# Performance work log

Hardware: AMD Instinct MI355X
Metric: run time of the kernel (lower is better)

## Reference

```python
import jax, jax.numpy as jnp
import numpy as np
import math

EMB, QK, V, HEAD = 512, 64, 64, 8
B, S = 8, 2048

def setup_inputs() -> dict:
    key = jax.random.key(0)
    ks = jax.random.split(key, 10)
    sc = 1.0 / math.sqrt(EMB)
    return {
        "x_q": jax.random.normal(ks[0], (B, S, EMB), jnp.float32),
        "x_k_v": jax.random.normal(ks[1], (B, S, EMB), jnp.float32),
        "attn_mask": jax.random.randint(ks[2], (B, S, S), 0, 2, jnp.int32),
        "w_q": jax.random.normal(ks[3], (HEAD * QK, EMB), jnp.float32) * sc,
        "b_q": jax.random.normal(ks[4], (HEAD * QK,), jnp.float32) * sc,
        "w_k": jax.random.normal(ks[5], (HEAD * QK, EMB), jnp.float32) * sc,
        "b_k": jax.random.normal(ks[6], (HEAD * QK,), jnp.float32) * sc,
        "w_v": jax.random.normal(ks[7], (HEAD * V, EMB), jnp.float32) * sc,
        "b_v": jax.random.normal(ks[8], (HEAD * V,), jnp.float32) * sc,
    }

def reference(x_q, x_k_v, attn_mask, w_q, b_q, w_k, b_k, w_v, b_v):
    Bq, Sq, _ = x_q.shape
    Skv = x_k_v.shape[1]
    # linear projections (torch Linear: x @ W.T + b)
    q = (x_q @ w_q.T + b_q).reshape(Bq, Sq, HEAD, QK)     # [B,Sq,H,Dk]
    k = (x_k_v @ w_k.T + b_k).reshape(Bq, Skv, HEAD, QK)  # [B,Skv,H,Dk]
    v = (x_k_v @ w_v.T + b_v).reshape(Bq, Skv, HEAD, V)   # [B,Skv,H,Dv]
    # scores [B,H,Sq,Skv]
    attn = jnp.einsum("bqhd,bkhd->bhqk", q, k) / math.sqrt(QK)
    mask = attn_mask[:, None, :, :].astype(bool)
    attn = jnp.where(mask, jnp.float32(-1e9), attn)
    attn = jax.nn.softmax(attn, axis=-1)
    z = jnp.einsum("bhqk,bkhd->bqhd", attn, v)            # [B,Sq,H,Dv]
    return z.reshape(Bq, Sq, HEAD * V)
```

## Files before the change

### kernel.cpp

```cpp
#include <hip/hip_runtime.h>
#include <hip/hip_bf16.h>
#include <math.h>

typedef float  f32x4  __attribute__((ext_vector_type(4)));
typedef float  f32x16 __attribute__((ext_vector_type(16)));
typedef short  s16x8  __attribute__((ext_vector_type(8)));
typedef __bf16 bf16x8 __attribute__((ext_vector_type(8)));
typedef unsigned int u32;
typedef unsigned int u32x4 __attribute__((ext_vector_type(4)));
typedef unsigned short u16;
typedef unsigned long long u64;

#define DEVI static __device__ __forceinline__

#if defined(__has_builtin) && __has_builtin(__builtin_amdgcn_exp2f)
#define EXP2(x) __builtin_amdgcn_exp2f(x)
#else
#define EXP2(x) exp2f(x)
#endif

DEVI u32 cvtpk(float lo, float hi) {
  u32 r;
  asm("v_cvt_pk_bf16_f32 %0, %1, %2" : "=v"(r) : "v"(lo), "v"(hi));
  return r;
}

DEVI f32x4 mfma_bf16(s16x8 a, s16x8 b, f32x4 c) {
  return __builtin_amdgcn_mfma_f32_16x16x32_bf16(
      __builtin_bit_cast(bf16x8, a), __builtin_bit_cast(bf16x8, b), c, 0, 0, 0);
}

DEVI f32x16 mfma32(s16x8 a, s16x8 b, f32x16 c) {
  return __builtin_amdgcn_mfma_f32_32x32x16_bf16(
      __builtin_bit_cast(bf16x8, a), __builtin_bit_cast(bf16x8, b), c, 0, 0, 0);
}

DEVI void gload_lds16(const void* g, void* l) {
  __builtin_amdgcn_global_load_lds(
      (const __attribute__((address_space(1))) void*)g,
      (__attribute__((address_space(3))) void*)l, 16, 0, 0);
}

__global__ __launch_bounds__(256)
void mask_pack(const int* __restrict__ mask, u64* __restrict__ mp) {
  const int t = threadIdx.x, lane = t & 63;
  const int gw = blockIdx.x * 4 + (t >> 6);
  const int kt = gw & 31, q = (gw >> 5) & 2047, b = gw >> 16;
  int mv = mask[((size_t)b * 2048 + q) * 2048 + kt * 64 + lane];
  u64 bits = __ballot(mv == 0);
  if (lane == 0) mp[((size_t)b * 32 + kt) * 2048 + q] = bits;
}

__global__ __launch_bounds__(256, 2)
void qkv_proj(const float* __restrict__ xq, const float* __restrict__ xkv,
              const float* __restrict__ wq, const float* __restrict__ bq,
              const float* __restrict__ wk, const float* __restrict__ bk,
              const float* __restrict__ wv, const float* __restrict__ bv,
              u16* __restrict__ Qo, u16* __restrict__ Ko, u16* __restrict__ VTo)
{
  __shared__ __align__(16) char smem[128 * 272];
  char* lds_a = smem;
  char* lds_b = smem + 8192;

  const int t = threadIdx.x, lane = t & 63, w = t >> 6;
  const int z = blockIdx.z;
  const float* X  = (z == 0) ? xq : xkv;
  const float* W  = (z == 0) ? wq : (z == 1 ? wk : wv);
  const float* Bv = (z == 0) ? bq : (z == 1 ? bk : bv);

  const int m0 = blockIdx.x * 128, n0 = blockIdx.y * 128;
  const int wr = w >> 1, wc = w & 1, g = lane >> 4, q15 = lane & 15;
  const int srow = t >> 1, shalf = t & 1;

  f32x4 acc[4][4];
  #pragma unroll
  for (int i = 0; i < 4; ++i)
    #pragma unroll
    for (int j = 0; j < 4; ++j) acc[i][j] = (f32x4){0.f, 0.f, 0.f, 0.f};

  const float* gA = X + (size_t)(m0 + srow) * 512 + shalf * 16;
  const float* gB = W + (size_t)(n0 + srow) * 512 + shalf * 16;
  const int wbyte = srow * 64;
  const int sw = (srow & 3) << 4;

  #pragma unroll 1
  for (int kt = 0; kt < 16; ++kt) {
    float4 fa[4], fb[4];
    #pragma unroll
    for (int j = 0; j < 4; ++j) {
      fa[j] = *(const float4*)(gA + kt * 32 + j * 4);
      fb[j] = *(const float4*)(gB + kt * 32 + j * 4);
    }
    __syncthreads();
    const float* pfa = (const float*)fa;
    const float* pfb = (const float*)fb;
    #pragma unroll
    for (int half = 0; half < 2; ++half) {
      u32x4 wa, wb;
      #pragma unroll
      for (int e2 = 0; e2 < 4; ++e2) {
        wa[e2] = cvtpk(pfa[half * 8 + 2 * e2], pfa[half * 8 + 2 * e2 + 1]);
        wb[e2] = cvtpk(pfb[half * 8 + 2 * e2], pfb[half * 8 + 2 * e2 + 1]);
      }
      *(u32x4*)(lds_a + wbyte + ((shalf * 32 + half * 16) ^ sw)) = wa;
      *(u32x4*)(lds_b + wbyte + ((shalf * 32 + half * 16) ^ sw)) = wb;
    }
    __syncthreads();
    s16x8 afr[4], bfr[4];
    #pragma unroll
    for (int mi = 0; mi < 4; ++mi) {
      int row = wr * 64 + mi * 16 + q15;
      afr[mi] = *(const s16x8*)(lds_a + row * 64 + ((g * 16) ^ ((row & 3) << 4)));
    }
    #pragma unroll
    for (int ni = 0; ni < 4; ++ni) {
      int row = wc * 64 + ni * 16 + q15;
      bfr[ni] = *(const s16x8*)(lds_b + row * 64 + ((g * 16) ^ ((row & 3) << 4)));
    }
    #pragma unroll
    for (int mi = 0; mi < 4; ++mi)
      #pragma unroll
      for (int ni = 0; ni < 4; ++ni)
        acc[mi][ni] = mfma_bf16(afr[mi], bfr[ni], acc[mi][ni]);
  }

  float bias[4];
  #pragma unroll
  for (int ni = 0; ni < 4; ++ni) bias[ni] = Bv[n0 + wc * 64 + ni * 16 + q15];

  if (z < 2) {
    u16* Out = z ? Ko : Qo;
    const float scale = z ? 1.0f : 0.18033688011112042f;
    #pragma unroll
    for (int mi = 0; mi < 4; ++mi)
      #pragma unroll
      for (int ni = 0; ni < 4; ++ni)
        #pragma unroll
        for (int r = 0; r < 4; r += 2) {
          int m = m0 + wr * 64 + mi * 16 + g * 4 + r;
          int n = n0 + wc * 64 + ni * 16 + q15;
          u32 pk = cvtpk((acc[mi][ni][r] + bias[ni]) * scale,
                         (acc[mi][ni][r + 1] + bias[ni]) * scale);
          Out[(size_t)m * 512 + n]       = (u16)pk;
          Out[(size_t)(m + 1) * 512 + n] = (u16)(pk >> 16);
        }
  } else {
    __syncthreads();
    #pragma unroll
    for (int mi = 0; mi < 4; ++mi)
      #pragma unroll
      for (int ni = 0; ni < 4; ++ni)
        #pragma unroll
        for (int r = 0; r < 4; r += 2) {
          int ml = wr * 64 + mi * 16 + g * 4 + r;
          int nl = wc * 64 + ni * 16 + q15;
          *(u32*)(smem + nl * 272 + ml * 2) =
              cvtpk(acc[mi][ni][r] + bias[ni], acc[mi][ni][r + 1] + bias[ni]);
        }
    __syncthreads();
    const int b  = m0 >> 11;
    const int s0 = m0 & 2047;
    #pragma unroll
    for (int nn = 0; nn < 2; ++nn) {
      int n  = nn * 64 + (t >> 2);
      int q4 = t & 3;
      u16* dst = VTo + (size_t)(b * 512 + n0 + n) * 2048 + s0 + q4 * 32;
      #pragma unroll
      for (int jj = 0; jj < 4; ++jj)
        *(s16x8*)(dst + jj * 8) = *(const s16x8*)(smem + n * 272 + q4 * 64 + jj * 16);
    }
  }
}

__global__ __launch_bounds__(128, 2)
void attn_fwd(const u16* __restrict__ Q, const u16* __restrict__ K,
              const u16* __restrict__ VT, const u64* __restrict__ MP,
              float* __restrict__ out)
{
  __shared__ __align__(16) char lds_k[2][8192];
  __shared__ __align__(16) char lds_v[2][8192];

  const int bid = blockIdx.x;
  const int h = bid & 7, b = (bid >> 3) & 7, qt = bid >> 6;
  const int t = threadIdx.x, lane = t & 63, w = t >> 6;
  const int l31 = lane & 31, hi = lane >> 5;
  const int qbase = qt * 128 + w * 64;
  const int swz = (l31 & 7) << 4;

  s16x8 qfa[4], qfb[4];
  #pragma unroll
  for (int j = 0; j < 4; ++j) {
    qfa[j] = *(const s16x8*)(Q + (size_t)(b * 2048 + qbase + l31) * 512
                               + h * 64 + j * 16 + hi * 8);
    qfb[j] = *(const s16x8*)(Q + (size_t)(b * 2048 + qbase + 32 + l31) * 512
                               + h * 64 + j * 16 + hi * 8);
  }
  asm volatile("" ::: "memory");

  f32x16 oA0 = {0.f,0.f,0.f,0.f,0.f,0.f,0.f,0.f,0.f,0.f,0.f,0.f,0.f,0.f,0.f,0.f};
  f32x16 oA1 = oA0, oB0 = oA0, oB1 = oA0, zA = oA0, zB = oA0;
  const f32x16 ZZ = oA0;
  const s16x8 onesf = {0x3F80,0x3F80,0x3F80,0x3F80,0x3F80,0x3F80,0x3F80,0x3F80};

  const int srow8 = lane >> 3, slot = lane & 7;
  const int sx = (slot ^ srow8) * 8;
  const u16* kPtr[4];
  const u16* vPtr[4];
  #pragma unroll
  for (int i = 0; i < 4; ++i) {
    int rl = w * 32 + i * 8 + srow8;
    kPtr[i] = K  + (size_t)(b * 2048 + rl) * 512 + h * 64 + sx;
    vPtr[i] = VT + (size_t)(b * 512 + h * 64 + rl) * 2048 + sx;
  }
  const u64* mpP = MP + (size_t)b * 32 * 2048 + qbase + l31;

  #pragma unroll
  for (int i = 0; i < 4; ++i) gload_lds16(kPtr[i], &lds_k[0][(w * 4 + i) * 1024]);
  #pragma unroll
  for (int i = 0; i < 4; ++i) gload_lds16(vPtr[i], &lds_v[0][(w * 4 + i) * 1024]);
  asm volatile("" ::: "memory");
  u64 pm0 = mpP[0], pm1 = mpP[32];

  #pragma unroll 1
  for (int kt = 0; kt < 32; ++kt) {
    const int cur = kt & 1;
    const u64 kwA = pm0, kwB = pm1;
    asm volatile("s_waitcnt vmcnt(0) lgkmcnt(0)" ::: "memory");
    __builtin_amdgcn_sched_barrier(0);
    asm volatile("s_barrier" ::: "memory");
    if (kt + 1 < 32) {
      #pragma unroll
      for (int i = 0; i < 4; ++i) { kPtr[i] += 32768; vPtr[i] += 64; }
      mpP += 2048;
      #pragma unroll
      for (int i = 0; i < 4; ++i) gload_lds16(kPtr[i], &lds_k[cur ^ 1][(w * 4 + i) * 1024]);
      #pragma unroll
      for (int i = 0; i < 4; ++i) gload_lds16(vPtr[i], &lds_v[cur ^ 1][(w * 4 + i) * 1024]);
      asm volatile("" ::: "memory");
      pm0 = mpP[0]; pm1 = mpP[32];
    }

    f32x16 pa0 = ZZ, pa1 = ZZ, pb0 = ZZ, pb1 = ZZ;
    __builtin_amdgcn_s_setprio(1);
    #pragma unroll
    for (int j = 0; j < 4; ++j) {
      s16x8 k0 = *(const s16x8*)(&lds_k[cur][ l31       * 128 + ((j * 32 + hi * 16) ^ swz)]);
      s16x8 k1 = *(const s16x8*)(&lds_k[cur][(l31 + 32) * 128 + ((j * 32 + hi * 16) ^ swz)]);
      pa0 = mfma32(k0, qfa[j], pa0);
      pa1 = mfma32(k1, qfa[j], pa1);
      pb0 = mfma32(k0, qfb[j], pb0);
      pb1 = mfma32(k1, qfb[j], pb1);
    }
    __builtin_amdgcn_s_setprio(0);

    u32 wa[16], wb[16];
    {
      u64 kws = kwA >> (hi * 4);
      u32 mm0 = (u32)kws, mm1 = (u32)(kws >> 32);
      #pragma unroll
      for (int t2 = 0; t2 < 2; ++t2) {
        const u32 mmw = t2 ? mm1 : mm0;
        #pragma unroll
        for (int q2 = 0; q2 < 8; ++q2) {
          const int bp = 8 * (q2 >> 1) + 2 * (q2 & 1);
          float s0v = t2 ? pa1[2 * q2] : pa0[2 * q2];
          float s1v = t2 ? pa1[2 * q2 + 1] : pa0[2 * q2 + 1];
          float e0 = EXP2(s0v), e1 = EXP2(s1v);
          u32 k0 = (u32)((int)(mmw << (31 - bp)) >> 31);
          u32 k1 = (u32)((int)(mmw << (30 - bp)) >> 31);
          e0 = __builtin_bit_cast(float, __builtin_bit_cast(u32, e0) & k0);
          e1 = __builtin_bit_cast(float, __builtin_bit_cast(u32, e1) & k1);
          wa[t2 * 8 + q2] = cvtpk(e0, e1);
        }
      }
    }
    {
      u64 kws = kwB >> (hi * 4);
      u32 mm0 = (u32)kws, mm1 = (u32)(kws >> 32);
      #pragma unroll
      for (int t2 = 0; t2 < 2; ++t2) {
        const u32 mmw = t2 ? mm1 : mm0;
        #pragma unroll
        for (int q2 = 0; q2 < 8; ++q2) {
          const int bp = 8 * (q2 >> 1) + 2 * (q2 & 1);
          float s0v = t2 ? pb1[2 * q2] : pb0[2 * q2];
          float s1v = t2 ? pb1[2 * q2 + 1] : pb0[2 * q2 + 1];
          float e0 = EXP2(s0v), e1 = EXP2(s1v);
          u32 k0 = (u32)((int)(mmw << (31 - bp)) >> 31);
          u32 k1 = (u32)((int)(mmw << (30 - bp)) >> 31);
          e0 = __builtin_bit_cast(float, __builtin_bit_cast(u32, e0) & k0);
          e1 = __builtin_bit_cast(float, __builtin_bit_cast(u32, e1) & k1);
          wb[t2 * 8 + q2] = cvtpk(e0, e1);
        }
      }
    }

    __builtin_amdgcn_s_setprio(1);
    #pragma unroll
    for (int j = 0; j < 4; ++j) {
      const int ia = 2 * j, ib = 2 * j + 1;
      u32 a0 = wa[(ia >> 2) * 8 + 2 * (ia & 3)];
      u32 a1 = wa[(ia >> 2) * 8 + 2 * (ia & 3) + 1];
      u32 a2 = wa[(ib >> 2) * 8 + 2 * (ib & 3)];
      u32 a3 = wa[(ib >> 2) * 8 + 2 * (ib & 3) + 1];
      asm("v_permlane32_swap_b32 %0, %1" : "+v"(a0), "+v"(a2));
      asm("v_permlane32_swap_b32 %0, %1" : "+v"(a1), "+v"(a3));
      u32x4 awA = {a0, a1, a2, a3};
      s16x8 afA = __builtin_bit_cast(s16x8, awA);
      u32 b0 = wb[(ia >> 2) * 8 + 2 * (ia & 3)];
      u32 b1 = wb[(ia >> 2) * 8 + 2 * (ia & 3) + 1];
      u32 b2 = wb[(ib >> 2) * 8 + 2 * (ib & 3)];
      u32 b3 = wb[(ib >> 2) * 8 + 2 * (ib & 3) + 1];
      asm("v_permlane32_swap_b32 %0, %1" : "+v"(b0), "+v"(b2));
      asm("v_permlane32_swap_b32 %0, %1" : "+v"(b1), "+v"(b3));
      u32x4 awB = {b0, b1, b2, b3};
      s16x8 afB = __builtin_bit_cast(s16x8, awB);
      s16x8 v0 = *(const s16x8*)(&lds_v[cur][ l31       * 128 + ((j * 32 + hi * 16) ^ swz)]);
      s16x8 v1 = *(const s16x8*)(&lds_v[cur][(l31 + 32) * 128 + ((j * 32 + hi * 16) ^ swz)]);
      oA0 = mfma32(afA, v0, oA0);
      oA1 = mfma32(afA, v1, oA1);
      zA  = mfma32(afA, onesf, zA);
      oB0 = mfma32(afB, v0, oB0);
      oB1 = mfma32(afB, v1, oB1);
      zB  = mfma32(afB, onesf, zB);
    }
    __builtin_amdgcn_s_setprio(0);
  }

  #pragma unroll
  for (int reg = 0; reg < 16; ++reg) {
    const int ql = (reg & 3) + 8 * (reg >> 2) + 4 * hi;
    float liA = 1.0f / zA[reg];
    float* po = out + (size_t)(b * 2048 + qbase + ql) * 512 + h * 64 + l31;
    po[0]  = oA0[reg] * liA;
    po[32] = oA1[reg] * liA;
    float liB = 1.0f / zB[reg];
    float* po2 = po + (size_t)32 * 512;
    po2[0]  = oB0[reg] * liB;
    po2[32] = oB1[reg] * liB;
  }
}

extern "C" void kernel_launch(void* const* d_in, const int* in_sizes, int n_in,
                              void* d_out, int out_size, void* d_ws, size_t ws_size,
                              hipStream_t stream) {
  const float* xq  = (const float*)d_in[0];
  const float* xkv = (const float*)d_in[1];
  const int*   msk = (const int*)d_in[2];
  const float* wq  = (const float*)d_in[3];
  const float* bq  = (const float*)d_in[4];
  const float* wk  = (const float*)d_in[5];
  const float* bk  = (const float*)d_in[6];
  const float* wv  = (const float*)d_in[7];
  const float* bv  = (const float*)d_in[8];

  u16* Qw = (u16*)d_ws;
  u16* Kw = Qw + (size_t)16384 * 512;
  u16* VT = Kw + (size_t)16384 * 512;
  u64* MP = (u64*)(VT + (size_t)4096 * 2048);

  mask_pack<<<dim3(131072), 256, 0, stream>>>(msk, MP);
  qkv_proj<<<dim3(128, 4, 3), 256, 0, stream>>>(xq, xkv, wq, bq, wk, bk, wv, bv,
                                                Qw, Kw, VT);
  attn_fwd<<<dim3(1024), 128, 0, stream>>>(Qw, Kw, VT, MP, (float*)d_out);
}
```

Measured before the change: 230.5 us.

## Load K into registers, give each wave private V buffers, drop block barriers

K fragments now come straight from global memory into registers, double-buffered across even and odd iterations. V tiles are staged into per-wave LDS buffers, so the per-iteration block-wide s_barrier is no longer needed and partial vmcnt waits let loads overlap compute. The softmax denominator is built from a scalar running sum of the masked exponentials, combined with a cross-lane shuffle, instead of extra MFMAs against a ones vector. Trade-offs are higher register pressure from holding two sets of K fragments and duplicated V loads per wave, which doubles global V traffic per block.

```diff
diff --git a/kernel.cpp b/kernel.cpp
--- a/kernel.cpp
+++ b/kernel.cpp
@@ -172,13 +172,68 @@
   }
 }
 
+DEVI void exp_pack(const f32x16& p0, const f32x16& p1, u64 kw, int hi,
+                   u32* wds, float& lrun) {
+  u64 kws = kw >> (hi * 4);
+  u32 mm0 = (u32)kws, mm1 = (u32)(kws >> 32);
+  float ls = 0.f;
+  #pragma unroll
+  for (int t2 = 0; t2 < 2; ++t2) {
+    const u32 mmw = t2 ? mm1 : mm0;
+    #pragma unroll
+    for (int q2 = 0; q2 < 8; ++q2) {
+      const int bp = 8 * (q2 >> 1) + 2 * (q2 & 1);
+      float s0v = t2 ? p1[2 * q2] : p0[2 * q2];
+      float s1v = t2 ? p1[2 * q2 + 1] : p0[2 * q2 + 1];
+      float e0 = EXP2(s0v), e1 = EXP2(s1v);
+      u32 k0 = (u32)((int)(mmw << (31 - bp)) >> 31);
+      u32 k1 = (u32)((int)(mmw << (30 - bp)) >> 31);
+      e0 = __builtin_bit_cast(float, __builtin_bit_cast(u32, e0) & k0);
+      e1 = __builtin_bit_cast(float, __builtin_bit_cast(u32, e1) & k1);
+      ls += e0; ls += e1;
+      wds[t2 * 8 + q2] = cvtpk(e0, e1);
+    }
+  }
+  lrun += ls;
+}
+
+DEVI void pv_accum(const u32* wa, const u32* wb, const char* vbase,
+                   int l31, int hi, int swz,
+                   f32x16& oA0, f32x16& oA1, f32x16& oB0, f32x16& oB1) {
+  #pragma unroll
+  for (int j = 0; j < 4; ++j) {
+    const int ia = 2 * j, ib = 2 * j + 1;
+    u32 a0 = wa[(ia >> 2) * 8 + 2 * (ia & 3)];
+    u32 a1 = wa[(ia >> 2) * 8 + 2 * (ia & 3) + 1];
+    u32 a2 = wa[(ib >> 2) * 8 + 2 * (ib & 3)];
+    u32 a3 = wa[(ib >> 2) * 8 + 2 * (ib & 3) + 1];
+    asm("v_permlane32_swap_b32 %0, %1" : "+v"(a0), "+v"(a2));
+    asm("v_permlane32_swap_b32 %0, %1" : "+v"(a1), "+v"(a3));
+    u32x4 awA = {a0, a1, a2, a3};
+    s16x8 afA = __builtin_bit_cast(s16x8, awA);
+    u32 b0 = wb[(ia >> 2) * 8 + 2 * (ia & 3)];
+    u32 b1 = wb[(ia >> 2) * 8 + 2 * (ia & 3) + 1];
+    u32 b2 = wb[(ib >> 2) * 8 + 2 * (ib & 3)];
+    u32 b3 = wb[(ib >> 2) * 8 + 2 * (ib & 3) + 1];
+    asm("v_permlane32_swap_b32 %0, %1" : "+v"(b0), "+v"(b2));
+    asm("v_permlane32_swap_b32 %0, %1" : "+v"(b1), "+v"(b3));
+    u32x4 awB = {b0, b1, b2, b3};
+    s16x8 afB = __builtin_bit_cast(s16x8, awB);
+    s16x8 v0 = *(const s16x8*)(vbase + l31 * 128        + ((j * 32 + hi * 16) ^ swz));
+    s16x8 v1 = *(const s16x8*)(vbase + (l31 + 32) * 128 + ((j * 32 + hi * 16) ^ swz));
+    oA0 = mfma32(afA, v0, oA0);
+    oA1 = mfma32(afA, v1, oA1);
+    oB0 = mfma32(afB, v0, oB0);
+    oB1 = mfma32(afB, v1, oB1);
+  }
+}
+
 __global__ __launch_bounds__(128, 2)
 void attn_fwd(const u16* __restrict__ Q, const u16* __restrict__ K,
               const u16* __restrict__ VT, const u64* __restrict__ MP,
               float* __restrict__ out)
 {
-  __shared__ __align__(16) char lds_k[2][8192];
-  __shared__ __align__(16) char lds_v[2][8192];
+  __shared__ __align__(16) char lds_v[2][2][8192];
 
   const int bid = blockIdx.x;
   const int h = bid & 7, b = (bid >> 3) & 7, qt = bid >> 6;
@@ -198,143 +253,95 @@
   asm volatile("" ::: "memory");
 
   f32x16 oA0 = {0.f,0.f,0.f,0.f,0.f,0.f,0.f,0.f,0.f,0.f,0.f,0.f,0.f,0.f,0.f,0.f};
-  f32x16 oA1 = oA0, oB0 = oA0, oB1 = oA0, zA = oA0, zB = oA0;
+  f32x16 oA1 = oA0, oB0 = oA0, oB1 = oA0;
   const f32x16 ZZ = oA0;
-  const s16x8 onesf = {0x3F80,0x3F80,0x3F80,0x3F80,0x3F80,0x3F80,0x3F80,0x3F80};
-
-  const int srow8 = lane >> 3, slot = lane & 7;
-  const int sx = (slot ^ srow8) * 8;
-  const u16* kPtr[4];
-  const u16* vPtr[4];
-  #pragma unroll
-  for (int i = 0; i < 4; ++i) {
-    int rl = w * 32 + i * 8 + srow8;
-    kPtr[i] = K  + (size_t)(b * 2048 + rl) * 512 + h * 64 + sx;
-    vPtr[i] = VT + (size_t)(b * 512 + h * 64 + rl) * 2048 + sx;
-  }
-  const u64* mpP = MP + (size_t)b * 32 * 2048 + qbase + l31;
-
-  #pragma unroll
-  for (int i = 0; i < 4; ++i) gload_lds16(kPtr[i], &lds_k[0][(w * 4 + i) * 1024]);
-  #pragma unroll
-  for (int i = 0; i < 4; ++i) gload_lds16(vPtr[i], &lds_v[0][(w * 4 + i) * 1024]);
-  asm volatile("" ::: "memory");
-  u64 pm0 = mpP[0], pm1 = mpP[32];
+  float lrunA = 0.f, lrunB = 0.f;
+
+  const char* kR0 = (const char*)K + ((size_t)(b * 2048 + l31) * 512 + h * 64) * 2 + hi * 16;
+  const char* kR1 = kR0 + 32 * 1024;
+  const int sx = ((lane & 7) ^ (lane >> 3)) * 8;
+  const u16* vB = VT + (size_t)(b * 512 + h * 64 + (lane >> 3)) * 2048 + sx;
+  const u64* mpA = MP + (size_t)b * 32 * 2048 + qbase + l31;
+  const u64* mpB = mpA + 32;
+
+  s16x8 kfE[8], kfO[8];
+  u64 pmEA, pmEB, pmOA, pmOB;
+
+  #pragma unroll
+  for (int i = 0; i < 8; ++i) gload_lds16(vB + i * 16384, &lds_v[w][0][i * 1024]);
+  asm volatile("" ::: "memory");
+  #pragma unroll
+  for (int j = 0; j < 4; ++j) {
+    kfE[j]     = *(const s16x8*)(kR0 + j * 32);
+    kfE[4 + j] = *(const s16x8*)(kR1 + j * 32);
+  }
+  kR0 += 65536; kR1 += 65536;
+  asm volatile("" ::: "memory");
+  pmEA = mpA[0]; pmEB = mpB[0]; mpA += 2048; mpB += 2048;
+  asm volatile("" ::: "memory");
+  #pragma unroll
+  for (int i = 0; i < 8; ++i) gload_lds16(vB + 64 + i * 16384, &lds_v[w][1][i * 1024]);
+  vB += 128;
+  asm volatile("" ::: "memory");
+
+#define BODY(KF, KFN, PMA_, PMB_, PMNA_, PMNB_, BUF, DO_K, DO_M, DO_V, WAITASM) do { \
+    f32x16 pa0 = ZZ, pa1 = ZZ, pb0 = ZZ, pb1 = ZZ;                                   \
+    _Pragma("unroll")                                                                 \
+    for (int j = 0; j < 4; ++j) {                                                     \
+      pa0 = mfma32(KF[j],     qfa[j], pa0);                                           \
+      pa1 = mfma32(KF[4 + j], qfa[j], pa1);                                           \
+      pb0 = mfma32(KF[j],     qfb[j], pb0);                                           \
+      pb1 = mfma32(KF[4 + j], qfb[j], pb1);                                           \
+    }                                                                                 \
+    if (DO_K) {                                                                       \
+      _Pragma("unroll")                                                               \
+      for (int j = 0; j < 4; ++j) {                                                   \
+        KFN[j]     = *(const s16x8*)(kR0 + j * 32);                                   \
+        KFN[4 + j] = *(const s16x8*)(kR1 + j * 32);                                   \
+      }                                                                               \
+      kR0 += 65536; kR1 += 65536;                                                     \
+      asm volatile("" ::: "memory");                                                  \
+    }                                                                                 \
+    if (DO_M) {                                                                       \
+      PMNA_ = mpA[0]; PMNB_ = mpB[0]; mpA += 2048; mpB += 2048;                       \
+      asm volatile("" ::: "memory");                                                  \
+    }                                                                                 \
+    u32 wa[16], wb[16];                                                               \
+    exp_pack(pa0, pa1, PMA_, hi, wa, lrunA);                                          \
+    exp_pack(pb0, pb1, PMB_, hi, wb, lrunB);                                          \
+    asm volatile("s_waitcnt " WAITASM ::: "memory");                                  \
+    pv_accum(wa, wb, &lds_v[w][BUF][0], l31, hi, swz, oA0, oA1, oB0, oB1);            \
+    asm volatile("s_waitcnt lgkmcnt(0)" ::: "memory");                                \
+    __builtin_amdgcn_sched_barrier(0);                                                \
+    if (DO_V) {                                                                       \
+      _Pragma("unroll")                                                               \
+      for (int i = 0; i < 8; ++i) gload_lds16(vB + i * 16384, &lds_v[w][BUF][i * 1024]); \
+      vB += 64;                                                                       \
+      asm volatile("" ::: "memory");                                                  \
+    }                                                                                 \
+  } while (0)
 
   #pragma unroll 1
-  for (int kt = 0; kt < 32; ++kt) {
-    const int cur = kt & 1;
-    const u64 kwA = pm0, kwB = pm1;
-    asm volatile("s_waitcnt vmcnt(0) lgkmcnt(0)" ::: "memory");
-    __builtin_amdgcn_sched_barrier(0);
-    asm volatile("s_barrier" ::: "memory");
-    if (kt + 1 < 32) {
-      #pragma unroll
-      for (int i = 0; i < 4; ++i) { kPtr[i] += 32768; vPtr[i] += 64; }
-      mpP += 2048;
-      #pragma unroll
-      for (int i = 0; i < 4; ++i) gload_lds16(kPtr[i], &lds_k[cur ^ 1][(w * 4 + i) * 1024]);
-      #pragma unroll
-      for (int i = 0; i < 4; ++i) gload_lds16(vPtr[i], &lds_v[cur ^ 1][(w * 4 + i) * 1024]);
-      asm volatile("" ::: "memory");
-      pm0 = mpP[0]; pm1 = mpP[32];
-    }
-
-    f32x16 pa0 = ZZ, pa1 = ZZ, pb0 = ZZ, pb1 = ZZ;
-    __builtin_amdgcn_s_setprio(1);
-    #pragma unroll
-    for (int j = 0; j < 4; ++j) {
-      s16x8 k0 = *(const s16x8*)(&lds_k[cur][ l31       * 128 + ((j * 32 + hi * 16) ^ swz)]);
-      s16x8 k1 = *(const s16x8*)(&lds_k[cur][(l31 + 32) * 128 + ((j * 32 + hi * 16) ^ swz)]);
-      pa0 = mfma32(k0, qfa[j], pa0);
-      pa1 = mfma32(k1, qfa[j], pa1);
-      pb0 = mfma32(k0, qfb[j], pb0);
-      pb1 = mfma32(k1, qfb[j], pb1);
-    }
-    __builtin_amdgcn_s_setprio(0);
-
-    u32 wa[16], wb[16];
-    {
-      u64 kws = kwA >> (hi * 4);
-      u32 mm0 = (u32)kws, mm1 = (u32)(kws >> 32);
-      #pragma unroll
-      for (int t2 = 0; t2 < 2; ++t2) {
-        const u32 mmw = t2 ? mm1 : mm0;
-        #pragma unroll
-        for (int q2 = 0; q2 < 8; ++q2) {
-          const int bp = 8 * (q2 >> 1) + 2 * (q2 & 1);
-          float s0v = t2 ? pa1[2 * q2] : pa0[2 * q2];
-          float s1v = t2 ? pa1[2 * q2 + 1] : pa0[2 * q2 + 1];
-          float e0 = EXP2(s0v), e1 = EXP2(s1v);
-          u32 k0 = (u32)((int)(mmw << (31 - bp)) >> 31);
-          u32 k1 = (u32)((int)(mmw << (30 - bp)) >> 31);
-          e0 = __builtin_bit_cast(float, __builtin_bit_cast(u32, e0) & k0);
-          e1 = __builtin_bit_cast(float, __builtin_bit_cast(u32, e1) & k1);
-          wa[t2 * 8 + q2] = cvtpk(e0, e1);
-        }
-      }
-    }
-    {
-      u64 kws = kwB >> (hi * 4);
-      u32 mm0 = (u32)kws, mm1 = (u32)(kws >> 32);
-      #pragma unroll
-      for (int t2 = 0; t2 < 2; ++t2) {
-        const u32 mmw = t2 ? mm1 : mm0;
-        #pragma unroll
-        for (int q2 = 0; q2 < 8; ++q2) {
-          const int bp = 8 * (q2 >> 1) + 2 * (q2 & 1);
-          float s0v = t2 ? pb1[2 * q2] : pb0[2 * q2];
-          float s1v = t2 ? pb1[2 * q2 + 1] : pb0[2 * q2 + 1];
-          float e0 = EXP2(s0v), e1 = EXP2(s1v);
-          u32 k0 = (u32)((int)(mmw << (31 - bp)) >> 31);
-          u32 k1 = (u32)((int)(mmw << (30 - bp)) >> 31);
-          e0 = __builtin_bit_cast(float, __builtin_bit_cast(u32, e0) & k0);
-          e1 = __builtin_bit_cast(float, __builtin_bit_cast(u32, e1) & k1);
-          wb[t2 * 8 + q2] = cvtpk(e0, e1);
-        }
-      }
-    }
-
-    __builtin_amdgcn_s_setprio(1);
-    #pragma unroll
-    for (int j = 0; j < 4; ++j) {
-      const int ia = 2 * j, ib = 2 * j + 1;
-      u32 a0 = wa[(ia >> 2) * 8 + 2 * (ia & 3)];
-      u32 a1 = wa[(ia >> 2) * 8 + 2 * (ia & 3) + 1];
-      u32 a2 = wa[(ib >> 2) * 8 + 2 * (ib & 3)];
-      u32 a3 = wa[(ib >> 2) * 8 + 2 * (ib & 3) + 1];
-      asm("v_permlane32_swap_b32 %0, %1" : "+v"(a0), "+v"(a2));
-      asm("v_permlane32_swap_b32 %0, %1" : "+v"(a1), "+v"(a3));
-      u32x4 awA = {a0, a1, a2, a3};
-      s16x8 afA = __builtin_bit_cast(s16x8, awA);
-      u32 b0 = wb[(ia >> 2) * 8 + 2 * (ia & 3)];
-      u32 b1 = wb[(ia >> 2) * 8 + 2 * (ia & 3) + 1];
-      u32 b2 = wb[(ib >> 2) * 8 + 2 * (ib & 3)];
-      u32 b3 = wb[(ib >> 2) * 8 + 2 * (ib & 3) + 1];
-      asm("v_permlane32_swap_b32 %0, %1" : "+v"(b0), "+v"(b2));
-      asm("v_permlane32_swap_b32 %0, %1" : "+v"(b1), "+v"(b3));
-      u32x4 awB = {b0, b1, b2, b3};
-      s16x8 afB = __builtin_bit_cast(s16x8, awB);
-      s16x8 v0 = *(const s16x8*)(&lds_v[cur][ l31       * 128 + ((j * 32 + hi * 16) ^ swz)]);
-      s16x8 v1 = *(const s16x8*)(&lds_v[cur][(l31 + 32) * 128 + ((j * 32 + hi * 16) ^ swz)]);
-      oA0 = mfma32(afA, v0, oA0);
-      oA1 = mfma32(afA, v1, oA1);
-      zA  = mfma32(afA, onesf, zA);
-      oB0 = mfma32(afB, v0, oB0);
-      oB1 = mfma32(afB, v1, oB1);
-      zB  = mfma32(afB, onesf, zB);
-    }
-    __builtin_amdgcn_s_setprio(0);
-  }
-
+  for (int kt2 = 0; kt2 < 15; ++kt2) {
+    BODY(kfE, kfO, pmEA, pmEB, pmOA, pmOB, 0, 1, 1, 1, "vmcnt(28)");
+    BODY(kfO, kfE, pmOA, pmOB, pmEA, pmEB, 1, 1, 1, 1, "vmcnt(28)");
+  }
+  BODY(kfE, kfO, pmEA, pmEB, pmOA, pmOB, 0, 1, 1, 0, "vmcnt(28)");
+  BODY(kfO, kfE, pmOA, pmOB, pmEA, pmEB, 1, 0, 0, 0, "vmcnt(10)");
+#undef BODY
+
+  lrunA += __shfl_xor(lrunA, 32);
+  lrunB += __shfl_xor(lrunB, 32);
+  const float rqA = 1.0f / lrunA;
+  const float rqB = 1.0f / lrunB;
   #pragma unroll
   for (int reg = 0; reg < 16; ++reg) {
     const int ql = (reg & 3) + 8 * (reg >> 2) + 4 * hi;
-    float liA = 1.0f / zA[reg];
+    const float liA = __shfl(rqA, ql);
+    const float liB = __shfl(rqB, ql);
     float* po = out + (size_t)(b * 2048 + qbase + ql) * 512 + h * 64 + l31;
     po[0]  = oA0[reg] * liA;
     po[32] = oA1[reg] * liA;
-    float liB = 1.0f / zB[reg];
     float* po2 = po + (size_t)32 * 512;
     po2[0]  = oB0[reg] * liB;
     po2[32] = oB1[reg] * liB;
```

Measured after the change: 298.9 us. 29.7% more time.
